# Kernel optimization log

Measured on AMD Instinct MI355X. Metric: run time of the kernel, lower is better.

Reference implementation:

```python
import jax, jax.numpy as jnp
import numpy as np

EPS = 1e-5
NUM_HEADS = 8


def setup_inputs() -> dict:
    key = jax.random.key(0)
    ks = jax.random.split(key, 4)
    B, C, H, W = 16, 512, 32, 32
    x = jax.random.normal(ks[0], (B, C, H, W), dtype=jnp.float32)
    gn_w = jnp.ones((C,), dtype=jnp.float32)
    gn_b = jnp.zeros((C,), dtype=jnp.float32)
    # 1x1 conv weights stored as [out_ch, in_ch] (kernel dims squeezed)
    qkv_w = jax.random.normal(ks[1], (3 * C, C), dtype=jnp.float32) * (1.0 / np.sqrt(C))
    qkv_b = jnp.zeros((3 * C,), dtype=jnp.float32)
    proj_w = jax.random.normal(ks[2], (C, C), dtype=jnp.float32) * (1.0 / np.sqrt(C))
    proj_b = jnp.zeros((C,), dtype=jnp.float32)
    return {"x": x, "gn_w": gn_w, "gn_b": gn_b, "qkv_w": qkv_w,
            "qkv_b": qkv_b, "proj_w": proj_w, "proj_b": proj_b}


def _group_norm(x, w, b, groups):
    B, C, H, W = x.shape
    xg = x.reshape(B, groups, C // groups, H, W)
    mu = jnp.mean(xg, axis=(2, 3, 4), keepdims=True)
    var = jnp.var(xg, axis=(2, 3, 4), keepdims=True)
    xn = ((xg - mu) * jax.lax.rsqrt(var + EPS)).reshape(B, C, H, W)
    return xn * w[None, :, None, None] + b[None, :, None, None]


def reference(x, gn_w, gn_b, qkv_w, qkv_b, proj_w, proj_b):
    B, C, H, W = x.shape
    heads = NUM_HEADS
    d = C // heads
    residual = x
    xn = _group_norm(x, gn_w, gn_b, heads)
    # 1x1 conv == channel matmul
    qkv = jnp.einsum('oc,bchw->bohw', qkv_w, xn) + qkv_b[None, :, None, None]
    q, k, v = jnp.split(qkv, 3, axis=1)  # each [B, C, H, W]
    q = q.reshape(B, heads, d, H * W)
    k = k.reshape(B, heads, d, H * W)
    v = v.reshape(B, heads, d, H * W)
    scale = 1.0 / np.sqrt(d).astype(np.float32)
    attn = jnp.einsum('bhcn,bhcm->bhnm', q, k) * scale  # [B,h,N,N]
    attn = jax.nn.softmax(attn, axis=-1)
    out = jnp.einsum('bhnm,bhcm->bhcn', attn, v).reshape(B, C, H, W)
    out = jnp.einsum('oc,bchw->bohw', proj_w, out) + proj_b[None, :, None, None]
    return residual + out
```

## Files before the change

### kernel.cpp

```cpp
#include <hip/hip_runtime.h>
#include <hip/hip_bf16.h>
#include <math.h>

typedef short bf16x8 __attribute__((ext_vector_type(8)));
typedef float f32x4  __attribute__((ext_vector_type(4)));
#define MFMA16(a,b,c) __builtin_amdgcn_mfma_f32_16x16x32_bf16(a,b,c,0,0,0)

#define EPSF 1e-5f
#define QSC 0.18033688f

#if __has_builtin(__builtin_amdgcn_exp2f)
#define EXP2(x) __builtin_amdgcn_exp2f(x)
#else
#define EXP2(x) exp2f(x)
#endif

__device__ __forceinline__ unsigned int pk2n(float a, float b){
  __hip_bfloat162 h = __float22bfloat162_rn(make_float2(a, b));
  return *reinterpret_cast<unsigned int*>(&h);
}
__device__ __forceinline__ unsigned short bfn(float f){
  __hip_bfloat16 h = __float2bfloat16(f);
  return *reinterpret_cast<unsigned short*>(&h);
}
__device__ __forceinline__ float4 ld4(const float* p){ return *reinterpret_cast<const float4*>(p); }

__device__ __forceinline__ void gl_lds16(const unsigned short* g, unsigned short* l){
  __builtin_amdgcn_global_load_lds(
      (const __attribute__((address_space(1))) unsigned int*)g,
      (__attribute__((address_space(3))) unsigned int*)l, 16, 0, 0);
}

__global__ __launch_bounds__(512) void pre_k(const float* __restrict__ x,
                                             const float* __restrict__ gnw,
                                             const float* __restrict__ gnb,
                                             unsigned short* __restrict__ xnT,
                                             const float* __restrict__ qkvw,
                                             const float* __restrict__ projw,
                                             unsigned int* __restrict__ wqb,
                                             unsigned int* __restrict__ wpb){
  __shared__ float Xl[2][64*65];
  __shared__ float red[16];
  int blk = blockIdx.x;
  int tid = threadIdx.x;
  if(blk >= 128){
    const float* src; unsigned int* dst; int base;
    if(blk < 320){ src = qkvw; dst = wqb; base = 128; }
    else         { src = projw; dst = wpb; base = 320; }
    int i = (blk - base)*1024 + tid*2;
    #pragma unroll
    for(int j = 0; j < 2; j++){
      float4 v = reinterpret_cast<const float4*>(src)[i + j];
      uint2 r; r.x = pk2n(v.x, v.y); r.y = pk2n(v.z, v.w);
      reinterpret_cast<uint2*>(dst)[i + j] = r;
    }
    return;
  }
  int b = blk >> 3, g = blk & 7;
  const float4* p4 = reinterpret_cast<const float4*>(x + (size_t)blk * 65536);
  float s1 = 0.f, s2 = 0.f;
  for(int i = tid; i < 16384; i += 512){
    float4 v = p4[i];
    s1 += (v.x + v.y) + (v.z + v.w);
    s2 += v.x*v.x + v.y*v.y + v.z*v.z + v.w*v.w;
  }
  #pragma unroll
  for(int off = 32; off; off >>= 1){ s1 += __shfl_xor(s1, off); s2 += __shfl_xor(s2, off); }
  if((tid & 63) == 0){ red[tid >> 6] = s1; red[8 + (tid >> 6)] = s2; }
  __syncthreads();
  float a = 0.f, b2 = 0.f;
  #pragma unroll
  for(int w = 0; w < 8; w++){ a += red[w]; b2 += red[8 + w]; }
  float mean = a * (1.f / 65536.f);
  float rstd = rsqrtf(b2 * (1.f / 65536.f) - mean * mean + EPSF);
  int half = tid >> 8, t256 = tid & 255;
  int nq = t256 & 15, rr = t256 >> 4;
  int c0 = g * 64;
  for(int it = 0; it < 8; it++){
    int n0 = (it*2 + half) * 64;
    __syncthreads();
    #pragma unroll
    for(int p = 0; p < 4; p++){
      int cl = p * 16 + rr, c = c0 + cl;
      float s = rstd * gnw[c], t = gnb[c] - mean * s;
      float4 v = ld4(x + ((size_t)(b*512 + c))*1024 + n0 + 4*nq);
      Xl[half][(4*nq+0)*65 + cl] = v.x*s + t;
      Xl[half][(4*nq+1)*65 + cl] = v.y*s + t;
      Xl[half][(4*nq+2)*65 + cl] = v.z*s + t;
      Xl[half][(4*nq+3)*65 + cl] = v.w*s + t;
    }
    __syncthreads();
    int n = t256 >> 2, cq = t256 & 3;
    float f[16];
    #pragma unroll
    for(int k = 0; k < 16; k++) f[k] = Xl[half][n*65 + 16*cq + k];
    uint4 w0, w1;
    w0.x = pk2n(f[0],f[1]);  w0.y = pk2n(f[2],f[3]);  w0.z = pk2n(f[4],f[5]);  w0.w = pk2n(f[6],f[7]);
    w1.x = pk2n(f[8],f[9]);  w1.y = pk2n(f[10],f[11]);w1.z = pk2n(f[12],f[13]);w1.w = pk2n(f[14],f[15]);
    unsigned short* dp = xnT + ((size_t)(b*1024 + n0 + n))*512 + c0 + 16*cq;
    *reinterpret_cast<uint4*>(dp)     = w0;
    *reinterpret_cast<uint4*>(dp + 8) = w1;
  }
}


__global__ __launch_bounds__(256) void qkv_mm(const unsigned short* __restrict__ A,
                                              const unsigned short* __restrict__ Bx,
                                              const float* __restrict__ bias,
                                              unsigned short* __restrict__ T,
                                              unsigned short* __restrict__ V){
  __shared__ __align__(16) unsigned short As[128*64], Bs[128*64];
  int tid = threadIdx.x;
  int n0 = blockIdx.x*128, o0 = blockIdx.y*128, b = blockIdx.z;
  int wid = tid >> 6, wr = wid >> 1, wc = wid & 1, ln = tid & 15, g = (tid >> 4) & 3;
  int l = tid & 63;
  int rsw = (ln & 7) << 3;
  int srow = 32*wid + (l >> 3);
  int scol = (((l & 7) ^ (l >> 3)) << 3);
  const unsigned short* Ag = A  + (size_t)(o0 + srow)*512 + scol;
  const unsigned short* Bg = Bx + ((size_t)(b*1024 + n0 + srow))*512 + scol;
  unsigned short* Asw = As + (32*wid)*64;
  unsigned short* Bsw = Bs + (32*wid)*64;
  f32x4 acc[4][4] = {};
  for(int k0 = 0; k0 < 512; k0 += 64){
    __syncthreads();
    #pragma unroll
    for(int c = 0; c < 4; c++){
      gl_lds16(Ag + (size_t)(8*c)*512 + k0, Asw + (8*c)*64);
      gl_lds16(Bg + (size_t)(8*c)*512 + k0, Bsw + (8*c)*64);
    }
    __syncthreads();
    #pragma unroll
    for(int kh = 0; kh < 2; kh++){
      int ro = (kh*32 + 8*g) ^ rsw;
      bf16x8 af[4], bfv[4];
      #pragma unroll
      for(int mf = 0; mf < 4; mf++)
        af[mf] = *reinterpret_cast<const bf16x8*>(&As[(wr*64 + 16*mf + ln)*64 + ro]);
      #pragma unroll
      for(int nf = 0; nf < 4; nf++)
        bfv[nf] = *reinterpret_cast<const bf16x8*>(&Bs[(wc*64 + 16*nf + ln)*64 + ro]);
      #pragma unroll
      for(int mf = 0; mf < 4; mf++)
        #pragma unroll
        for(int nf = 0; nf < 4; nf++)
          acc[mf][nf] = MFMA16(af[mf], bfv[nf], acc[mf][nf]);
    }
  }
  int obase = o0 + wr*64, nbase = n0 + wc*64;
  __syncthreads();
  unsigned short* scr = (wid < 2 ? As : Bs) + (wid & 1) * 2560;
  float sc = (obase < 512) ? QSC : 1.0f;
  if(obase < 1024){
    #pragma unroll
    for(int h2 = 0; h2 < 2; h2++){
      asm volatile("s_waitcnt lgkmcnt(0)" ::: "memory");
      __builtin_amdgcn_sched_barrier(0);
      #pragma unroll
      for(int mf2 = 0; mf2 < 2; mf2++){
        int mf = 2*h2 + mf2;
        int og = obase + 16*mf + 4*g;
        float b0 = bias[og], b1 = bias[og+1], b2 = bias[og+2], b3 = bias[og+3];
        #pragma unroll
        for(int nf = 0; nf < 4; nf++){
          uint2 pr;
          pr.x = pk2n((acc[mf][nf][0]+b0)*sc, (acc[mf][nf][1]+b1)*sc);
          pr.y = pk2n((acc[mf][nf][2]+b2)*sc, (acc[mf][nf][3]+b3)*sc);
          *reinterpret_cast<uint2*>(&scr[(16*nf + ln)*40 + 16*mf2 + 4*g]) = pr;
        }
      }
      asm volatile("s_waitcnt lgkmcnt(0)" ::: "memory");
      __builtin_amdgcn_sched_barrier(0);
      const unsigned short* rp = &scr[l*40];
      uint4 r0 = *reinterpret_cast<const uint4*>(rp);
      uint4 r1 = *reinterpret_cast<const uint4*>(rp+8);
      uint4 r2 = *reinterpret_cast<const uint4*>(rp+16);
      uint4 r3 = *reinterpret_cast<const uint4*>(rp+24);
      unsigned short* dp = T + ((size_t)(b*1024 + nbase + l))*1024 + obase + 32*h2;
      *reinterpret_cast<uint4*>(dp)    = r0;
      *reinterpret_cast<uint4*>(dp+8)  = r1;
      *reinterpret_cast<uint4*>(dp+16) = r2;
      *reinterpret_cast<uint4*>(dp+24) = r3;
    }
  } else {
    #pragma unroll
    for(int h2 = 0; h2 < 2; h2++){
      asm volatile("s_waitcnt lgkmcnt(0)" ::: "memory");
      __builtin_amdgcn_sched_barrier(0);
      #pragma unroll
      for(int nf2 = 0; nf2 < 2; nf2++){
        int nf = 2*h2 + nf2;
        #pragma unroll
        for(int mf = 0; mf < 4; mf++){
          int og = obase + 16*mf + 4*g;
          #pragma unroll
          for(int r = 0; r < 4; r++)
            scr[(16*mf + 4*g + r)*40 + 16*nf2 + ln] = bfn(acc[mf][nf][r] + bias[og+r]);
        }
      }
      asm volatile("s_waitcnt lgkmcnt(0)" ::: "memory");
      __builtin_amdgcn_sched_barrier(0);
      const unsigned short* rp = &scr[l*40];
      uint4 r0 = *reinterpret_cast<const uint4*>(rp);
      uint4 r1 = *reinterpret_cast<const uint4*>(rp+8);
      uint4 r2 = *reinterpret_cast<const uint4*>(rp+16);
      uint4 r3 = *reinterpret_cast<const uint4*>(rp+24);
      unsigned short* dp = V + ((size_t)(b*512 + obase - 1024 + l))*1024 + nbase + 32*h2;
      *reinterpret_cast<uint4*>(dp)    = r0;
      *reinterpret_cast<uint4*>(dp+8)  = r1;
      *reinterpret_cast<uint4*>(dp+16) = r2;
      *reinterpret_cast<uint4*>(dp+24) = r3;
    }
  }
}

__global__ __launch_bounds__(256) void attn_bf_k(const unsigned short* __restrict__ T,
                                                 const unsigned short* __restrict__ V,
                                                 unsigned short* __restrict__ attT){
  __shared__ __align__(16) unsigned short KT[2][64*64];
  __shared__ __align__(16) unsigned short Vt[2][64*64];
  __shared__ __align__(16) unsigned int   Pl[4*16*32];
  int tid = threadIdx.x;
  int id = blockIdx.x;
  int bh = (id >> 7) * 8 + (id & 7);
  int n0 = ((id >> 3) & 15) * 64;
  int b = bh >> 3, h = bh & 7;
  int wq = tid >> 6, ln = tid & 15, g = (tid >> 4) & 3;
  int l = tid & 63;
  int nl = n0 + wq*16 + ln;
  const unsigned short* Tb = T + ((size_t)b << 20);
  bf16x8 qf0 = *reinterpret_cast<const bf16x8*>(Tb + (size_t)nl*1024 + h*64 + 8*g);
  bf16x8 qf1 = *reinterpret_cast<const bf16x8*>(Tb + (size_t)nl*1024 + h*64 + 32 + 8*g);
  f32x4 acc[4] = {};
  float l_part = 0.f;
  const unsigned short* kg = Tb + 512 + h*64;
  const unsigned short* vg = V + ((size_t)(b*512 + h*64))*1024;
  int pbase = wq*512 + ln*32;
  int psw = (ln & 7) << 2;
  int swz  = (((l & 7) << 3) ^ ((l >> 3) << 3));
  const unsigned short* ksrc = kg + (size_t)(wq*16 + (l>>3))*1024 + swz;
  const unsigned short* vsrc = vg + (size_t)(wq*16 + (l>>3))*1024 + swz;
  int rsw = (ln & 7) << 3;
  int ro0 = (8*g) ^ rsw, ro1 = (32 + 8*g) ^ rsw;
  {
    unsigned short* kb = &KT[0][wq*16*64];
    unsigned short* vb = &Vt[0][wq*16*64];
    gl_lds16(ksrc,            kb);
    gl_lds16(ksrc + 8*1024,   kb + 8*64);
    gl_lds16(vsrc,            vb);
    gl_lds16(vsrc + 8*1024,   vb + 8*64);
  }
  __syncthreads();
  for(int t = 0; t < 16; t++){
    int buf = t & 1;
    if(t < 15){
      int m1 = (t + 1) * 64;
      unsigned short* kb = &KT[buf^1][wq*16*64];
      unsigned short* vb = &Vt[buf^1][wq*16*64];
      gl_lds16(ksrc + (size_t)m1*1024,          kb);
      gl_lds16(ksrc + (size_t)(m1+8)*1024,      kb + 8*64);
      gl_lds16(vsrc + m1,                       vb);
      gl_lds16(vsrc + 8*1024 + m1,              vb + 8*64);
    }
    f32x4 sf[4];
    #pragma unroll
    for(int mf = 0; mf < 4; mf++){
      bf16x8 a0 = *reinterpret_cast<const bf16x8*>(&KT[buf][(16*mf + ln)*64 + ro0]);
      bf16x8 a1 = *reinterpret_cast<const bf16x8*>(&KT[buf][(16*mf + ln)*64 + ro1]);
      f32x4 z = {0.f, 0.f, 0.f, 0.f};
      z = MFMA16(a0, qf0, z);
      sf[mf] = MFMA16(a1, qf1, z);
    }
    float p[16];
    #pragma unroll
    for(int mf = 0; mf < 4; mf++)
      #pragma unroll
      for(int r = 0; r < 4; r++){
        float v = EXP2(sf[mf][r]);
        p[mf*4 + r] = v;
        l_part += v;
      }
    #pragma unroll
    for(int mt = 0; mt < 4; mt++){
      Pl[pbase + ((8*mt + 2*g + 0) ^ psw)] = pk2n(p[4*mt + 0], p[4*mt + 1]);
      Pl[pbase + ((8*mt + 2*g + 1) ^ psw)] = pk2n(p[4*mt + 2], p[4*mt + 3]);
    }
    asm volatile("s_waitcnt lgkmcnt(0)" ::: "memory");
    __builtin_amdgcn_sched_barrier(0);
    union { uint4 u; bf16x8 hv; } pb0, pb1;
    pb0.u = *reinterpret_cast<const uint4*>(&Pl[pbase + ((4*g) ^ psw)]);
    pb1.u = *reinterpret_cast<const uint4*>(&Pl[pbase + ((16 + 4*g) ^ psw)]);
    #pragma unroll
    for(int cf = 0; cf < 4; cf++){
      bf16x8 v0 = *reinterpret_cast<const bf16x8*>(&Vt[buf][(16*cf + ln)*64 + ro0]);
      bf16x8 v1 = *reinterpret_cast<const bf16x8*>(&Vt[buf][(16*cf + ln)*64 + ro1]);
      acc[cf] = MFMA16(v0, pb0.hv, acc[cf]);
      acc[cf] = MFMA16(v1, pb1.hv, acc[cf]);
    }
    __syncthreads();
  }
  float lsum = l_part;
  lsum += __shfl_xor(lsum, 16);
  lsum += __shfl_xor(lsum, 32);
  float inv = 1.f / lsum;
  unsigned short* op = attT + ((size_t)(b*1024 + nl))*512 + h*64;
  #pragma unroll
  for(int cf = 0; cf < 4; cf++){
    uint2 pr;
    pr.x = pk2n(acc[cf][0]*inv, acc[cf][1]*inv);
    pr.y = pk2n(acc[cf][2]*inv, acc[cf][3]*inv);
    *reinterpret_cast<uint2*>(op + 16*cf + 4*g) = pr;
  }
}

__global__ __launch_bounds__(256) void proj_mm(const unsigned short* __restrict__ A,
                                               const unsigned short* __restrict__ Bx,
                                               const float* __restrict__ bias,
                                               const float* __restrict__ resid,
                                               float* __restrict__ out){
  __shared__ __align__(16) unsigned short As[128*64], Bs[128*64];
  int tid = threadIdx.x;
  int n0 = blockIdx.x*128, o0 = blockIdx.y*128, b = blockIdx.z;
  int wid = tid >> 6, wr = wid >> 1, wc = wid & 1, ln = tid & 15, g = (tid >> 4) & 3;
  int l = tid & 63;
  int rsw = (ln & 7) << 3;
  int srow = 32*wid + (l >> 3);
  int scol = (((l & 7) ^ (l >> 3)) << 3);
  const unsigned short* Ag = A  + (size_t)(o0 + srow)*512 + scol;
  const unsigned short* Bg = Bx + ((size_t)(b*1024 + n0 + srow))*512 + scol;
  unsigned short* Asw = As + (32*wid)*64;
  unsigned short* Bsw = Bs + (32*wid)*64;
  f32x4 acc[4][4] = {};
  for(int k0 = 0; k0 < 512; k0 += 64){
    __syncthreads();
    #pragma unroll
    for(int c = 0; c < 4; c++){
      gl_lds16(Ag + (size_t)(8*c)*512 + k0, Asw + (8*c)*64);
      gl_lds16(Bg + (size_t)(8*c)*512 + k0, Bsw + (8*c)*64);
    }
    __syncthreads();
    #pragma unroll
    for(int kh = 0; kh < 2; kh++){
      int ro = (kh*32 + 8*g) ^ rsw;
      bf16x8 af[4], bfv[4];
      #pragma unroll
      for(int mf = 0; mf < 4; mf++)
        af[mf] = *reinterpret_cast<const bf16x8*>(&As[(wr*64 + 16*mf + ln)*64 + ro]);
      #pragma unroll
      for(int nf = 0; nf < 4; nf++)
        bfv[nf] = *reinterpret_cast<const bf16x8*>(&Bs[(wc*64 + 16*nf + ln)*64 + ro]);
      #pragma unroll
      for(int mf = 0; mf < 4; mf++)
        #pragma unroll
        for(int nf = 0; nf < 4; nf++)
          acc[mf][nf] = MFMA16(af[mf], bfv[nf], acc[mf][nf]);
    }
  }
  #pragma unroll
  for(int mf = 0; mf < 4; mf++)
    #pragma unroll
    for(int r = 0; r < 4; r++){
      int o = o0 + wr*64 + 16*mf + 4*g + r;
      float bo = bias[o];
      #pragma unroll
      for(int nf = 0; nf < 4; nf++){
        int n = n0 + wc*64 + 16*nf + ln;
        size_t off = ((size_t)(b*512 + o))*1024 + n;
        out[off] = acc[mf][nf][r] + bo + resid[off];
      }
    }
}

extern "C" void kernel_launch(void* const* d_in, const int* in_sizes, int n_in,
                              void* d_out, int out_size, void* d_ws, size_t ws_size,
                              hipStream_t stream){
  const float* x     = (const float*)d_in[0];
  const float* gnw   = (const float*)d_in[1];
  const float* gnb   = (const float*)d_in[2];
  const float* qkvw  = (const float*)d_in[3];
  const float* qkvb  = (const float*)d_in[4];
  const float* projw = (const float*)d_in[5];
  const float* projb = (const float*)d_in[6];
  float* out = (float*)d_out;

  char* w = (char*)d_ws;
  unsigned short* wqb = (unsigned short*)w;  w += (size_t)1536*512*2;
  unsigned short* wpb = (unsigned short*)w;  w += (size_t)512*512*2;
  unsigned short* xnT = (unsigned short*)w;  w += (size_t)16*1024*512*2;
  unsigned short* Tqk = (unsigned short*)w;  w += (size_t)16*1024*1024*2;
  unsigned short* Vb  = (unsigned short*)w;  w += (size_t)16*512*1024*2;
  unsigned short* attT = (unsigned short*)w; w += (size_t)16*1024*512*2;

  hipLaunchKernelGGL(pre_k, dim3(384), dim3(512), 0, stream,
                     x, gnw, gnb, xnT, qkvw, projw,
                     (unsigned int*)wqb, (unsigned int*)wpb);
  hipLaunchKernelGGL(qkv_mm, dim3(8, 12, 16), dim3(256), 0, stream, wqb, xnT, qkvb, Tqk, Vb);
  hipLaunchKernelGGL(attn_bf_k, dim3(2048), dim3(256), 0, stream, Tqk, Vb, attT);
  hipLaunchKernelGGL(proj_mm, dim3(8, 4, 16), dim3(256), 0, stream, wpb, attT, projb, x, out);
}
```

Measured before the change: 151.9 us.

## Double-buffer LDS tiles in QKV and projection GEMMs to overlap loads with MFMA

Both GEMM kernels now keep two LDS buffers and issue the global-to-LDS loads for the next K tile before computing on the current one. Explicit vmcnt waits and raw s_barrier replace the two __syncthreads per iteration. The intent is to hide global load latency behind the MFMA work. LDS use per block doubles to 64KB, which may lower occupancy, and the QKV epilogue scratch is remapped into the first A buffer.

```diff
diff --git a/kernel.cpp b/kernel.cpp
--- a/kernel.cpp
+++ b/kernel.cpp
@@ -109,7 +109,7 @@
                                               const float* __restrict__ bias,
                                               unsigned short* __restrict__ T,
                                               unsigned short* __restrict__ V){
-  __shared__ __align__(16) unsigned short As[128*64], Bs[128*64];
+  __shared__ __align__(16) unsigned short As[2][128*64], Bs[2][128*64];
   int tid = threadIdx.x;
   int n0 = blockIdx.x*128, o0 = blockIdx.y*128, b = blockIdx.z;
   int wid = tid >> 6, wr = wid >> 1, wc = wid & 1, ln = tid & 15, g = (tid >> 4) & 3;
@@ -119,37 +119,49 @@
   int scol = (((l & 7) ^ (l >> 3)) << 3);
   const unsigned short* Ag = A  + (size_t)(o0 + srow)*512 + scol;
   const unsigned short* Bg = Bx + ((size_t)(b*1024 + n0 + srow))*512 + scol;
-  unsigned short* Asw = As + (32*wid)*64;
-  unsigned short* Bsw = Bs + (32*wid)*64;
   f32x4 acc[4][4] = {};
-  for(int k0 = 0; k0 < 512; k0 += 64){
-    __syncthreads();
-    #pragma unroll
-    for(int c = 0; c < 4; c++){
-      gl_lds16(Ag + (size_t)(8*c)*512 + k0, Asw + (8*c)*64);
-      gl_lds16(Bg + (size_t)(8*c)*512 + k0, Bsw + (8*c)*64);
-    }
-    __syncthreads();
+  #pragma unroll
+  for(int c = 0; c < 4; c++){
+    gl_lds16(Ag + (size_t)(8*c)*512, &As[0][(32*wid + 8*c)*64]);
+    gl_lds16(Bg + (size_t)(8*c)*512, &Bs[0][(32*wid + 8*c)*64]);
+  }
+  for(int t = 0; t < 8; t++){
+    int buf = t & 1;
+    if(t < 7){
+      int k1 = (t + 1) * 64;
+      #pragma unroll
+      for(int c = 0; c < 4; c++){
+        gl_lds16(Ag + (size_t)(8*c)*512 + k1, &As[buf^1][(32*wid + 8*c)*64]);
+        gl_lds16(Bg + (size_t)(8*c)*512 + k1, &Bs[buf^1][(32*wid + 8*c)*64]);
+      }
+      asm volatile("s_waitcnt vmcnt(8)" ::: "memory");
+    } else {
+      asm volatile("s_waitcnt vmcnt(0)" ::: "memory");
+    }
+    __builtin_amdgcn_sched_barrier(0);
+    __builtin_amdgcn_s_barrier();
+    __builtin_amdgcn_sched_barrier(0);
     #pragma unroll
     for(int kh = 0; kh < 2; kh++){
       int ro = (kh*32 + 8*g) ^ rsw;
       bf16x8 af[4], bfv[4];
       #pragma unroll
       for(int mf = 0; mf < 4; mf++)
-        af[mf] = *reinterpret_cast<const bf16x8*>(&As[(wr*64 + 16*mf + ln)*64 + ro]);
+        af[mf] = *reinterpret_cast<const bf16x8*>(&As[buf][(wr*64 + 16*mf + ln)*64 + ro]);
       #pragma unroll
       for(int nf = 0; nf < 4; nf++)
-        bfv[nf] = *reinterpret_cast<const bf16x8*>(&Bs[(wc*64 + 16*nf + ln)*64 + ro]);
+        bfv[nf] = *reinterpret_cast<const bf16x8*>(&Bs[buf][(wc*64 + 16*nf + ln)*64 + ro]);
       #pragma unroll
       for(int mf = 0; mf < 4; mf++)
         #pragma unroll
         for(int nf = 0; nf < 4; nf++)
           acc[mf][nf] = MFMA16(af[mf], bfv[nf], acc[mf][nf]);
     }
+    __builtin_amdgcn_sched_barrier(0);
+    __builtin_amdgcn_s_barrier();
   }
   int obase = o0 + wr*64, nbase = n0 + wc*64;
-  __syncthreads();
-  unsigned short* scr = (wid < 2 ? As : Bs) + (wid & 1) * 2560;
+  unsigned short* scr = &As[0][0] + wid * 2560;
   float sc = (obase < 512) ? QSC : 1.0f;
   if(obase < 1024){
     #pragma unroll
@@ -318,7 +330,7 @@
                                                const float* __restrict__ bias,
                                                const float* __restrict__ resid,
                                                float* __restrict__ out){
-  __shared__ __align__(16) unsigned short As[128*64], Bs[128*64];
+  __shared__ __align__(16) unsigned short As[2][128*64], Bs[2][128*64];
   int tid = threadIdx.x;
   int n0 = blockIdx.x*128, o0 = blockIdx.y*128, b = blockIdx.z;
   int wid = tid >> 6, wr = wid >> 1, wc = wid & 1, ln = tid & 15, g = (tid >> 4) & 3;
@@ -328,33 +340,46 @@
   int scol = (((l & 7) ^ (l >> 3)) << 3);
   const unsigned short* Ag = A  + (size_t)(o0 + srow)*512 + scol;
   const unsigned short* Bg = Bx + ((size_t)(b*1024 + n0 + srow))*512 + scol;
-  unsigned short* Asw = As + (32*wid)*64;
-  unsigned short* Bsw = Bs + (32*wid)*64;
   f32x4 acc[4][4] = {};
-  for(int k0 = 0; k0 < 512; k0 += 64){
-    __syncthreads();
-    #pragma unroll
-    for(int c = 0; c < 4; c++){
-      gl_lds16(Ag + (size_t)(8*c)*512 + k0, Asw + (8*c)*64);
-      gl_lds16(Bg + (size_t)(8*c)*512 + k0, Bsw + (8*c)*64);
-    }
-    __syncthreads();
+  #pragma unroll
+  for(int c = 0; c < 4; c++){
+    gl_lds16(Ag + (size_t)(8*c)*512, &As[0][(32*wid + 8*c)*64]);
+    gl_lds16(Bg + (size_t)(8*c)*512, &Bs[0][(32*wid + 8*c)*64]);
+  }
+  for(int t = 0; t < 8; t++){
+    int buf = t & 1;
+    if(t < 7){
+      int k1 = (t + 1) * 64;
+      #pragma unroll
+      for(int c = 0; c < 4; c++){
+        gl_lds16(Ag + (size_t)(8*c)*512 + k1, &As[buf^1][(32*wid + 8*c)*64]);
+        gl_lds16(Bg + (size_t)(8*c)*512 + k1, &Bs[buf^1][(32*wid + 8*c)*64]);
+      }
+      asm volatile("s_waitcnt vmcnt(8)" ::: "memory");
+    } else {
+      asm volatile("s_waitcnt vmcnt(0)" ::: "memory");
+    }
+    __builtin_amdgcn_sched_barrier(0);
+    __builtin_amdgcn_s_barrier();
+    __builtin_amdgcn_sched_barrier(0);
     #pragma unroll
     for(int kh = 0; kh < 2; kh++){
       int ro = (kh*32 + 8*g) ^ rsw;
       bf16x8 af[4], bfv[4];
       #pragma unroll
       for(int mf = 0; mf < 4; mf++)
-        af[mf] = *reinterpret_cast<const bf16x8*>(&As[(wr*64 + 16*mf + ln)*64 + ro]);
+        af[mf] = *reinterpret_cast<const bf16x8*>(&As[buf][(wr*64 + 16*mf + ln)*64 + ro]);
       #pragma unroll
       for(int nf = 0; nf < 4; nf++)
-        bfv[nf] = *reinterpret_cast<const bf16x8*>(&Bs[(wc*64 + 16*nf + ln)*64 + ro]);
+        bfv[nf] = *reinterpret_cast<const bf16x8*>(&Bs[buf][(wc*64 + 16*nf + ln)*64 + ro]);
       #pragma unroll
       for(int mf = 0; mf < 4; mf++)
         #pragma unroll
         for(int nf = 0; nf < 4; nf++)
           acc[mf][nf] = MFMA16(af[mf], bfv[nf], acc[mf][nf]);
     }
+    __builtin_amdgcn_sched_barrier(0);
+    __builtin_amdgcn_s_barrier();
   }
   #pragma unroll
   for(int mf = 0; mf < 4; mf++)
```

Result: faster. 147.8 us, median of 2 (-2.7%).
